# Performance work log

Measured on AMD Instinct MI355X. Metric: run time of the kernel, lower is better.

The kernel has to match this reference:

```python
import jax, jax.numpy as jnp
import numpy as np

B, L, D, E, K, P = 1024, 320, 128, 8, 2, 96
NOISE_EPS = 0.01
LOSS_COEF = 0.01


def setup_inputs() -> dict:
    key = jax.random.key(0)
    ks = jax.random.split(key, 8)
    return {
        "x": jax.random.normal(ks[0], (B, L, D), jnp.float32),
        "x_mark_enc": jax.random.normal(ks[1], (B, L, 4), jnp.float32),
        "noise": jax.random.normal(ks[2], (B, E), jnp.float32),  # randn_like in torch
        "start_w": jax.random.normal(ks[3], (D, 1), jnp.float32) * 0.05,
        "start_b": jnp.zeros((1,), jnp.float32),
        "w_gate": jax.random.normal(ks[4], (L, E), jnp.float32) * 0.02,
        "w_noise": jax.random.normal(ks[5], (L, E), jnp.float32) * 0.02,
        "expert_w": jax.random.normal(ks[6], (E, L, P), jnp.float32) * (1.0 / np.sqrt(L)),
        "expert_b": jnp.zeros((E, P, D), jnp.float32),
    }


def _norm_cdf(v):
    return 0.5 * (1.0 + jax.lax.erf(v * (1.0 / np.sqrt(2.0)).astype(v.dtype) if hasattr((1.0 / np.sqrt(2.0)), 'astype') else v / jnp.sqrt(jnp.asarray(2.0, v.dtype))))


def _cdf(v):
    # standard normal CDF, Normal(0,1).cdf
    return 0.5 * (1.0 + jax.lax.erf(v / jnp.sqrt(jnp.asarray(2.0, v.dtype))))


def _cv_squared(v):
    eps = 1e-10
    return jnp.var(v, ddof=1) / (jnp.mean(v) ** 2 + eps)


def reference(x, x_mark_enc, noise, start_w, start_b, w_gate, w_noise, expert_b, expert_w):
    # --- noisy top-k gating (train mode) ---
    g = jnp.squeeze(x @ start_w, -1) + start_b  # [B, L]
    clean_logits = g @ w_gate                    # [B, E]
    noise_std = jax.nn.softplus(g @ w_noise) + NOISE_EPS
    noisy_logits = clean_logits + noise * noise_std

    top_logits, top_idx = jax.lax.top_k(noisy_logits, K + 1)  # [B, K+1]
    top_k_gates = jax.nn.softmax(top_logits[:, :K], axis=1)
    gates = jnp.zeros_like(noisy_logits).at[
        jnp.arange(noisy_logits.shape[0])[:, None], top_idx[:, :K]
    ].set(top_k_gates)  # [B, E] sparse gates (zeros elsewhere)

    # --- differentiable load via prob-in-top-k ---
    thr_in = top_logits[:, K:K + 1]       # (k+1)-th noisy value
    thr_out = top_logits[:, K - 1:K]      # k-th noisy value
    clean_c = jnp.where(jnp.isnan(clean_logits), 0.0, clean_logits)
    prob = jnp.where(
        noisy_logits > thr_in,
        _cdf((clean_c - thr_in) / noise_std),
        _cdf((clean_c - thr_out) / noise_std),
    )
    load = prob.sum(0)          # [E]
    importance = gates.sum(0)   # [E]
    balance_loss = LOSS_COEF * (_cv_squared(importance) + _cv_squared(load))

    # --- dispatch/combine: dense-equivalent of SparseDispatcher ---
    # expert e: out_e = einsum('bld,lp->bpd', x, W_e); combine weights = gates
    per_expert = jnp.einsum('bld,elp->ebpd', x, expert_w)          # [E, B, P, D]
    out = jnp.einsum('be,ebpd->bpd', gates, per_expert)
    out = out + jnp.einsum('be,epd->bpd', gates, expert_b)
    regu_sum = jnp.asarray(0.0, jnp.float32)
    return out, balance_loss, regu_sum
```

## Files before the change

### kernel.cpp

```cpp
#include <hip/hip_runtime.h>
#include <hip/hip_bf16.h>

#define Bn 1024
#define Lr 320
#define Dd 128
#define Ee 8
#define Pp 96

typedef short bf16x8 __attribute__((ext_vector_type(8)));
typedef float f32x4 __attribute__((ext_vector_type(4)));
typedef unsigned u32x4 __attribute__((ext_vector_type(4)));
typedef unsigned short u16;

__device__ __forceinline__ float cdf_f(float v) {
    return 0.5f * (1.0f + erff(v * 0.70710678118654752f));
}
__device__ __forceinline__ float softplus_f(float x) {
    return fmaxf(x, 0.0f) + log1pf(expf(-fabsf(x)));
}
__device__ __forceinline__ u16 f2bf(float f) {
    unsigned int u = __float_as_uint(f);
    return (u16)((u + 0x7fffu + ((u >> 16) & 1u)) >> 16);
}
__device__ __forceinline__ float bf2f(u16 u) {
    return __uint_as_float(((unsigned int)u) << 16);
}

__device__ __forceinline__ void gload16(const void* g, void* l) {
    __builtin_amdgcn_global_load_lds(
        (const __attribute__((address_space(1))) void*)g,
        (__attribute__((address_space(3))) void*)l, 16, 0, 0);
}

__global__ __launch_bounds__(256) void transpose_w(
    const float* __restrict__ ew, u16* __restrict__ wt)
{
    __shared__ float tile[Pp * 33];
    const int e  = blockIdx.x;
    const int l0 = blockIdx.y * 32;
    const int t  = threadIdx.x;
    #pragma unroll
    for (int i = 0; i < 12; ++i) {
        const int idx = t + 256 * i;
        const int lp = idx / 96, p = idx - 96 * lp;
        tile[p * 33 + lp] = ew[((size_t)e * Lr + l0 + lp) * Pp + p];
    }
    __syncthreads();
    #pragma unroll
    for (int i = 0; i < 6; ++i) {
        const int g = t + 256 * i;
        const int p = g >> 4, l2 = (g & 15) * 2;
        const unsigned pk = (unsigned)f2bf(tile[p * 33 + l2]) |
                            ((unsigned)f2bf(tile[p * 33 + l2 + 1]) << 16);
        *(unsigned*)&wt[((size_t)(e * Pp + p)) * Lr + l0 + l2] = pk;
    }
}

__global__ __launch_bounds__(256, 8) void g_kernel(
    const float* __restrict__ x, const float* __restrict__ start_w,
    const float* __restrict__ start_b, float* __restrict__ g_out)
{
    const int t  = threadIdx.x;
    const int lc = blockIdx.x;
    const int b  = blockIdx.y;
    const float sb = start_b[0];

    float4 sw[4];
    #pragma unroll
    for (int j = 0; j < 4; ++j) sw[j] = ((const float4*)start_w)[(t & 7) + 8 * j];

    const float* xb = x + ((size_t)b * Lr + lc * 64) * Dd;
    #pragma unroll
    for (int p2 = 0; p2 < 2; ++p2) {
        const int r = p2 * 32 + (t >> 3);
        float acc = 0.f;
        #pragma unroll
        for (int j = 0; j < 4; ++j) {
            const float4 v = ((const float4*)(xb + (size_t)r * Dd))[(t & 7) + 8 * j];
            acc += v.x * sw[j].x + v.y * sw[j].y + v.z * sw[j].z + v.w * sw[j].w;
        }
        #pragma unroll
        for (int off = 1; off <= 4; off <<= 1) acc += __shfl_xor(acc, off);
        if ((t & 7) == 0) g_out[(size_t)b * Lr + lc * 64 + r] = acc + sb;
    }
}

__global__ __launch_bounds__(256) void gate_kernel(
    const float* __restrict__ g, const float* __restrict__ noise,
    const float* __restrict__ w_gate, const float* __restrict__ w_noise,
    float* __restrict__ accum, float* __restrict__ gates_out)
{
    __shared__ float sred[16];
    const int t    = threadIdx.x;
    const int lane = t & 63;
    const int wv   = t >> 6;
    const int b    = blockIdx.x * 4 + wv;

    if (t < 16) sred[t] = 0.f;
    __syncthreads();

    const int e = lane & 7, seg = lane >> 3;
    const float* gb = g + (size_t)b * Lr;
    float pc = 0.f, pn = 0.f;
    #pragma unroll 8
    for (int i = 0; i < 40; ++i) {
        const int l = seg * 40 + i;
        const float gv = gb[l];
        pc += gv * w_gate[l * Ee + e];
        pn += gv * w_noise[l * Ee + e];
    }
    #pragma unroll
    for (int off = 8; off <= 32; off <<= 1) {
        pc += __shfl_xor(pc, off);
        pn += __shfl_xor(pn, off);
    }
    const float sdv   = softplus_f(pn) + 0.01f;
    float       c     = pc;
    const float nz    = noise[b * Ee + e];
    const float noisy = c + nz * sdv;

    float nv[8];
    #pragma unroll
    for (int j = 0; j < 8; ++j) nv[j] = __shfl(noisy, j);

    int i0 = -1, i1 = -1;
    float v0 = -INFINITY, v1 = -INFINITY, v2 = -INFINITY;
    #pragma unroll
    for (int i = 0; i < 8; ++i) if (nv[i] > v0) { v0 = nv[i]; i0 = i; }
    #pragma unroll
    for (int i = 0; i < 8; ++i) if (i != i0 && nv[i] > v1) { v1 = nv[i]; i1 = i; }
    #pragma unroll
    for (int i = 0; i < 8; ++i) if (i != i0 && i != i1 && nv[i] > v2) { v2 = nv[i]; }

    const float ex1 = expf(v1 - v0);
    const float den = 1.f + ex1;
    const float gate_e = (e == i0) ? (1.f / den) : ((e == i1) ? (ex1 / den) : 0.f);

    if (isnan(c)) c = 0.f;
    const float pr = (noisy > v2) ? cdf_f((c - v2) / sdv) : cdf_f((c - v1) / sdv);

    if (lane < 8) {
        gates_out[b * Ee + e] = gate_e;
        atomicAdd(&sred[8 + e], gate_e);
        atomicAdd(&sred[e], pr);
    }
    __syncthreads();
    if (t < 16) atomicAdd(&accum[t], sred[t]);
}

__global__ __launch_bounds__(256, 4) void mm_kernel(
    const float* __restrict__ x, const u16* __restrict__ wt,
    const float* __restrict__ expert_b, const float* __restrict__ gates,
    float* __restrict__ out)
{
    __shared__ __align__(16) float    Xs[2][32 * 64];
    __shared__ __align__(16) unsigned Ws[2][192 * 16];

    const int b    = blockIdx.x >> 1;
    const int h    = blockIdx.x & 1;
    const int tid  = threadIdx.x;
    const int lane = tid & 63;
    const int wv   = tid >> 6;
    const int quad = lane >> 4;
    const int r16  = lane & 15;

    int e0 = 0, e1 = 0; float g0 = 0.f, g1 = 0.f; int cnt = 0;
    #pragma unroll
    for (int e = 0; e < Ee; ++e) {
        const float gv = gates[b * Ee + e];
        if (gv != 0.f) {
            if (cnt == 0) { e0 = e; g0 = gv; }
            else if (cnt == 1) { e1 = e; g1 = gv; }
            ++cnt;
        }
    }

    const float* xb  = x + (size_t)b * Lr * Dd + h * 64;
    const u16*   w0r = wt + (size_t)e0 * Pp * Lr;
    const u16*   w1r = wt + (size_t)e1 * Pp * Lr;

    const int xrow = lane >> 4;
    const int xcol = lane & 15;
    const int wrow = lane >> 2;
    const int wq   = lane & 3;

    auto STAGE = [&](int buf, int l0) {
        #pragma unroll
        for (int i = 0; i < 2; ++i) {
            const int c  = 2 * wv + i;
            const int l  = 4 * c + xrow;
            const int sx = (((l >> 3) & 1) << 4) | (((l >> 3) & 2) << 1);
            const int d4 = (4 * xcol) ^ sx;
            gload16(xb + (size_t)(l0 + l) * Dd + d4, (void*)&Xs[buf][c * 256]);
        }
        #pragma unroll
        for (int i = 0; i < 3; ++i) {
            const int c  = 3 * wv + i;
            const int r  = 16 * c + wrow;
            const int dw = (4 * wq) ^ ((r & 3) << 2);
            const u16* src = (c < 6) ? (w0r + (size_t)r * Lr)
                                     : (w1r + (size_t)(r - 96) * Lr);
            gload16(src + l0 + 2 * dw, (void*)&Ws[buf][c * 256]);
        }
    };

    f32x4 a0[6], a1[6];
    #pragma unroll
    for (int m = 0; m < 6; ++m) {
        a0[m] = (f32x4){0.f, 0.f, 0.f, 0.f};
        a1[m] = (f32x4){0.f, 0.f, 0.f, 0.f};
    }

    const int sxq    = ((quad & 1) << 4) | ((quad & 2) << 1);
    const int xcolr  = (16 * wv + r16) ^ sxq;
    const int wdw    = (4 * quad) ^ ((r16 & 3) << 2);

    union UF { u32x4 q; bf16x8 v; unsigned u[4]; };

    STAGE(0, 0);
    __syncthreads();
    int cur = 0;
    for (int t = 0; t < 10; ++t) {
        if (t < 9) STAGE(cur ^ 1, 32 * (t + 1));
        float xv[8];
        #pragma unroll
        for (int k = 0; k < 8; ++k)
            xv[k] = Xs[cur][(8 * quad + k) * 64 + xcolr];
        UF xf;
        #pragma unroll
        for (int k2 = 0; k2 < 4; ++k2)
            xf.u[k2] = (unsigned)f2bf(xv[2 * k2]) |
                       ((unsigned)f2bf(xv[2 * k2 + 1]) << 16);
        #pragma unroll
        for (int m = 0; m < 6; ++m) {
            UF a0f, a1f;
            a0f.q = *(const u32x4*)&Ws[cur][(16 * m + r16) * 16 + wdw];
            a1f.q = *(const u32x4*)&Ws[cur][(96 + 16 * m + r16) * 16 + wdw];
            a0[m] = __builtin_amdgcn_mfma_f32_16x16x32_bf16(a0f.v, xf.v, a0[m], 0, 0, 0);
            a1[m] = __builtin_amdgcn_mfma_f32_16x16x32_bf16(a1f.v, xf.v, a1[m], 0, 0, 0);
        }
        __syncthreads();
        cur ^= 1;
    }

    const int d = h * 64 + 16 * wv + r16;
    const float* eb0 = expert_b + (size_t)e0 * Pp * Dd;
    const float* eb1 = expert_b + (size_t)e1 * Pp * Dd;
    #pragma unroll
    for (int m = 0; m < 6; ++m) {
        #pragma unroll
        for (int r = 0; r < 4; ++r) {
            const int p = 16 * m + 4 * quad + r;
            out[((size_t)b * Pp + p) * Dd + d] =
                g0 * (a0[m][r] + eb0[p * Dd + d]) +
                g1 * (a1[m][r] + eb1[p * Dd + d]);
        }
    }
}

__global__ void loss_kernel(const float* __restrict__ accum,
                            float* __restrict__ out_scalars)
{
    if (threadIdx.x == 0) {
        float lo[8], im[8];
        #pragma unroll
        for (int i = 0; i < 8; ++i) { lo[i] = accum[i]; im[i] = accum[8 + i]; }
        float ml = 0.f, mi = 0.f;
        #pragma unroll
        for (int i = 0; i < 8; ++i) { ml += lo[i]; mi += im[i]; }
        ml *= 0.125f; mi *= 0.125f;
        float sl = 0.f, si = 0.f;
        #pragma unroll
        for (int i = 0; i < 8; ++i) {
            const float dl = lo[i] - ml, di = im[i] - mi;
            sl += dl * dl; si += di * di;
        }
        const float cvl = (sl / 7.f) / (ml * ml + 1e-10f);
        const float cvi = (si / 7.f) / (mi * mi + 1e-10f);
        out_scalars[0] = 0.01f * (cvi + cvl);
        out_scalars[1] = 0.0f;
    }
}

extern "C" void kernel_launch(void* const* d_in, const int* in_sizes, int n_in,
                              void* d_out, int out_size, void* d_ws, size_t ws_size,
                              hipStream_t stream)
{
    const float* x        = (const float*)d_in[0];
    const float* noise    = (const float*)d_in[2];
    const float* start_w  = (const float*)d_in[3];
    const float* start_b  = (const float*)d_in[4];
    const float* w_gate   = (const float*)d_in[5];
    const float* w_noise  = (const float*)d_in[6];
    const float* expert_w = (const float*)d_in[7];
    const float* expert_b = (const float*)d_in[8];
    float* out            = (float*)d_out;

    float* accum = (float*)d_ws;
    float* gates = accum + 16;
    float* gbuf  = gates + Bn * Ee;
    u16*   wt    = (u16*)(gbuf + Bn * Lr);

    hipMemsetAsync(accum, 0, 16 * sizeof(float), stream);
    hipLaunchKernelGGL(transpose_w, dim3(Ee, Lr / 32), dim3(256), 0, stream,
                       expert_w, wt);
    hipLaunchKernelGGL(g_kernel, dim3(5, Bn), dim3(256), 0, stream,
                       x, start_w, start_b, gbuf);
    hipLaunchKernelGGL(gate_kernel, dim3(Bn / 4), dim3(256), 0, stream,
                       gbuf, noise, w_gate, w_noise, accum, gates);
    hipLaunchKernelGGL(mm_kernel, dim3(Bn * 2), dim3(256), 0, stream,
                       x, wt, expert_b, gates, out);
    hipLaunchKernelGGL(loss_kernel, dim3(1), dim3(64), 0, stream,
                       accum, out + (size_t)Bn * Pp * Dd);
}
```

Before: 311.8 us.

## Fuse gating projection, top-k gating, and expert matmul into one per-batch kernel

Replaces the separate g, gate, and matmul kernels with one kernel per batch row. Each block reads the full x slab once, computes the start projection and the gating from it, and keeps a bf16-converted, transposed copy of x in LDS for the MFMA loop. This removes the second read of x from HBM, the global round-trips for g and gates, and two launches. In exchange each block needs about 80KB of LDS and 512 threads, which lowers occupancy. Global atomics now run per block instead of per four rows.

```diff
diff --git a/kernel.cpp b/kernel.cpp
--- a/kernel.cpp
+++ b/kernel.cpp
@@ -56,153 +56,147 @@
     }
 }
 
-__global__ __launch_bounds__(256, 8) void g_kernel(
-    const float* __restrict__ x, const float* __restrict__ start_w,
-    const float* __restrict__ start_b, float* __restrict__ g_out)
-{
-    const int t  = threadIdx.x;
-    const int lc = blockIdx.x;
-    const int b  = blockIdx.y;
-    const float sb = start_b[0];
-
-    float4 sw[4];
-    #pragma unroll
-    for (int j = 0; j < 4; ++j) sw[j] = ((const float4*)start_w)[(t & 7) + 8 * j];
-
-    const float* xb = x + ((size_t)b * Lr + lc * 64) * Dd;
-    #pragma unroll
-    for (int p2 = 0; p2 < 2; ++p2) {
-        const int r = p2 * 32 + (t >> 3);
-        float acc = 0.f;
-        #pragma unroll
-        for (int j = 0; j < 4; ++j) {
-            const float4 v = ((const float4*)(xb + (size_t)r * Dd))[(t & 7) + 8 * j];
-            acc += v.x * sw[j].x + v.y * sw[j].y + v.z * sw[j].z + v.w * sw[j].w;
-        }
-        #pragma unroll
-        for (int off = 1; off <= 4; off <<= 1) acc += __shfl_xor(acc, off);
-        if ((t & 7) == 0) g_out[(size_t)b * Lr + lc * 64 + r] = acc + sb;
-    }
-}
-
-__global__ __launch_bounds__(256) void gate_kernel(
-    const float* __restrict__ g, const float* __restrict__ noise,
+__global__ __launch_bounds__(512) void fused_kernel(
+    const float* __restrict__ x, const u16* __restrict__ wt,
+    const float* __restrict__ expert_b, const float* __restrict__ noise,
     const float* __restrict__ w_gate, const float* __restrict__ w_noise,
-    float* __restrict__ accum, float* __restrict__ gates_out)
-{
-    __shared__ float sred[16];
+    const float* __restrict__ start_w, const float* __restrict__ start_b,
+    float* __restrict__ accum, float* __restrict__ out)
+{
+    __shared__ __align__(16) unsigned XT[10 * 128 * 16];
+    __shared__ __align__(16) unsigned Ws[2][192 * 16];
+    __shared__ __align__(8)  float gl[Lr];
+    __shared__ float gsh[2];
+    __shared__ int   ish[2];
+
+    const int b    = blockIdx.x;
     const int t    = threadIdx.x;
     const int lane = t & 63;
     const int wv   = t >> 6;
-    const int b    = blockIdx.x * 4 + wv;
-
-    if (t < 16) sred[t] = 0.f;
-    __syncthreads();
-
-    const int e = lane & 7, seg = lane >> 3;
-    const float* gb = g + (size_t)b * Lr;
-    float pc = 0.f, pn = 0.f;
-    #pragma unroll 8
-    for (int i = 0; i < 40; ++i) {
-        const int l = seg * 40 + i;
-        const float gv = gb[l];
-        pc += gv * w_gate[l * Ee + e];
-        pn += gv * w_noise[l * Ee + e];
-    }
-    #pragma unroll
-    for (int off = 8; off <= 32; off <<= 1) {
-        pc += __shfl_xor(pc, off);
-        pn += __shfl_xor(pn, off);
-    }
-    const float sdv   = softplus_f(pn) + 0.01f;
-    float       c     = pc;
-    const float nz    = noise[b * Ee + e];
-    const float noisy = c + nz * sdv;
-
-    float nv[8];
-    #pragma unroll
-    for (int j = 0; j < 8; ++j) nv[j] = __shfl(noisy, j);
-
-    int i0 = -1, i1 = -1;
-    float v0 = -INFINITY, v1 = -INFINITY, v2 = -INFINITY;
-    #pragma unroll
-    for (int i = 0; i < 8; ++i) if (nv[i] > v0) { v0 = nv[i]; i0 = i; }
-    #pragma unroll
-    for (int i = 0; i < 8; ++i) if (i != i0 && nv[i] > v1) { v1 = nv[i]; i1 = i; }
-    #pragma unroll
-    for (int i = 0; i < 8; ++i) if (i != i0 && i != i1 && nv[i] > v2) { v2 = nv[i]; }
-
-    const float ex1 = expf(v1 - v0);
-    const float den = 1.f + ex1;
-    const float gate_e = (e == i0) ? (1.f / den) : ((e == i1) ? (ex1 / den) : 0.f);
-
-    if (isnan(c)) c = 0.f;
-    const float pr = (noisy > v2) ? cdf_f((c - v2) / sdv) : cdf_f((c - v1) / sdv);
-
-    if (lane < 8) {
-        gates_out[b * Ee + e] = gate_e;
-        atomicAdd(&sred[8 + e], gate_e);
-        atomicAdd(&sred[e], pr);
-    }
-    __syncthreads();
-    if (t < 16) atomicAdd(&accum[t], sred[t]);
-}
-
-__global__ __launch_bounds__(256, 4) void mm_kernel(
-    const float* __restrict__ x, const u16* __restrict__ wt,
-    const float* __restrict__ expert_b, const float* __restrict__ gates,
-    float* __restrict__ out)
-{
-    __shared__ __align__(16) float    Xs[2][32 * 64];
-    __shared__ __align__(16) unsigned Ws[2][192 * 16];
-
-    const int b    = blockIdx.x >> 1;
-    const int h    = blockIdx.x & 1;
-    const int tid  = threadIdx.x;
-    const int lane = tid & 63;
-    const int wv   = tid >> 6;
-    const int quad = lane >> 4;
-    const int r16  = lane & 15;
-
-    int e0 = 0, e1 = 0; float g0 = 0.f, g1 = 0.f; int cnt = 0;
-    #pragma unroll
-    for (int e = 0; e < Ee; ++e) {
-        const float gv = gates[b * Ee + e];
-        if (gv != 0.f) {
-            if (cnt == 0) { e0 = e; g0 = gv; }
-            else if (cnt == 1) { e1 = e; g1 = gv; }
-            ++cnt;
-        }
-    }
-
-    const float* xb  = x + (size_t)b * Lr * Dd + h * 64;
-    const u16*   w0r = wt + (size_t)e0 * Pp * Lr;
-    const u16*   w1r = wt + (size_t)e1 * Pp * Lr;
-
-    const int xrow = lane >> 4;
-    const int xcol = lane & 15;
-    const int wrow = lane >> 2;
-    const int wq   = lane & 3;
-
-    auto STAGE = [&](int buf, int l0) {
+
+    const float sb = start_b[0];
+    const int f8 = t & 7;
+    float4 sw[4];
+    #pragma unroll
+    for (int j = 0; j < 4; ++j) sw[j] = ((const float4*)start_w)[f8 + 8 * j];
+
+    #pragma unroll
+    for (int pass = 0; pass < 3; ++pass) {
+        const int pi = (t >> 3) + 64 * pass;
+        if (pi < 160) {
+            const float* r0 = x + ((size_t)b * Lr + 2 * pi) * Dd;
+            float4 v0[4], v1[4];
+            #pragma unroll
+            for (int j = 0; j < 4; ++j) {
+                v0[j] = ((const float4*)r0)[f8 + 8 * j];
+                v1[j] = ((const float4*)(r0 + Dd))[f8 + 8 * j];
+            }
+            float a0 = 0.f, a1 = 0.f;
+            #pragma unroll
+            for (int j = 0; j < 4; ++j) {
+                a0 += v0[j].x * sw[j].x + v0[j].y * sw[j].y +
+                      v0[j].z * sw[j].z + v0[j].w * sw[j].w;
+                a1 += v1[j].x * sw[j].x + v1[j].y * sw[j].y +
+                      v1[j].z * sw[j].z + v1[j].w * sw[j].w;
+            }
+            #pragma unroll
+            for (int off = 1; off <= 4; off <<= 1) {
+                a0 += __shfl_xor(a0, off);
+                a1 += __shfl_xor(a1, off);
+            }
+            if (f8 == 0) { gl[2 * pi] = a0 + sb; gl[2 * pi + 1] = a1 + sb; }
+            const int tt = pi >> 4, k2 = pi & 15;
+            #pragma unroll
+            for (int j = 0; j < 4; ++j) {
+                const float* p0 = (const float*)&v0[j];
+                const float* p1 = (const float*)&v1[j];
+                #pragma unroll
+                for (int jj = 0; jj < 4; ++jj) {
+                    const int d  = 4 * (f8 + 8 * j) + jj;
+                    const int sg = ((d ^ (d >> 2)) & 3) << 2;
+                    XT[(tt * 128 + d) * 16 + (k2 ^ sg)] =
+                        (unsigned)f2bf(p0[jj]) | ((unsigned)f2bf(p1[jj]) << 16);
+                }
+            }
+        }
+    }
+    __syncthreads();
+
+    if (t < 64) {
+        const int e = t & 7, seg = t >> 3;
+        float pc = 0.f, pn = 0.f;
+        #pragma unroll 8
+        for (int i = 0; i < 40; ++i) {
+            const int l = seg * 40 + i;
+            const float gv = gl[l];
+            pc += gv * w_gate[l * Ee + e];
+            pn += gv * w_noise[l * Ee + e];
+        }
+        #pragma unroll
+        for (int off = 8; off <= 32; off <<= 1) {
+            pc += __shfl_xor(pc, off);
+            pn += __shfl_xor(pn, off);
+        }
+        const float sdv   = softplus_f(pn) + 0.01f;
+        float       c     = pc;
+        const float nz    = noise[b * Ee + e];
+        const float noisy = c + nz * sdv;
+
+        float nv[8];
+        #pragma unroll
+        for (int j = 0; j < 8; ++j) nv[j] = __shfl(noisy, j);
+
+        int i0 = -1, i1 = -1;
+        float v0 = -INFINITY, v1 = -INFINITY, v2 = -INFINITY;
+        #pragma unroll
+        for (int i = 0; i < 8; ++i) if (nv[i] > v0) { v0 = nv[i]; i0 = i; }
+        #pragma unroll
+        for (int i = 0; i < 8; ++i) if (i != i0 && nv[i] > v1) { v1 = nv[i]; i1 = i; }
+        #pragma unroll
+        for (int i = 0; i < 8; ++i) if (i != i0 && i != i1 && nv[i] > v2) { v2 = nv[i]; }
+
+        const float ex1 = expf(v1 - v0);
+        const float den = 1.f + ex1;
+        const float gate_e = (e == i0) ? (1.f / den) : ((e == i1) ? (ex1 / den) : 0.f);
+
+        if (isnan(c)) c = 0.f;
+        const float pr = (noisy > v2) ? cdf_f((c - v2) / sdv) : cdf_f((c - v1) / sdv);
+
+        if (t == 0) {
+            ish[0] = i0; ish[1] = i1;
+            gsh[0] = 1.f / den; gsh[1] = ex1 / den;
+        }
+        if (t < 8) {
+            atomicAdd(&accum[8 + e], gate_e);
+            atomicAdd(&accum[e], pr);
+        }
+    }
+    __syncthreads();
+
+    const int e0 = ish[0], e1 = ish[1];
+    const float g0 = gsh[0], g1 = gsh[1];
+    const u16* w0r = wt + (size_t)e0 * Pp * Lr;
+    const u16* w1r = wt + (size_t)e1 * Pp * Lr;
+
+    const int wrow = lane >> 2, wq = lane & 3;
+    auto STAGE_W = [&](int buf, int l0) {
         #pragma unroll
         for (int i = 0; i < 2; ++i) {
-            const int c  = 2 * wv + i;
-            const int l  = 4 * c + xrow;
-            const int sx = (((l >> 3) & 1) << 4) | (((l >> 3) & 2) << 1);
-            const int d4 = (4 * xcol) ^ sx;
-            gload16(xb + (size_t)(l0 + l) * Dd + d4, (void*)&Xs[buf][c * 256]);
-        }
-        #pragma unroll
-        for (int i = 0; i < 3; ++i) {
-            const int c  = 3 * wv + i;
-            const int r  = 16 * c + wrow;
-            const int dw = (4 * wq) ^ ((r & 3) << 2);
-            const u16* src = (c < 6) ? (w0r + (size_t)r * Lr)
-                                     : (w1r + (size_t)(r - 96) * Lr);
-            gload16(src + l0 + 2 * dw, (void*)&Ws[buf][c * 256]);
+            const int c = wv + 8 * i;
+            if (c < 12) {
+                const int r  = 16 * c + wrow;
+                const int dw = (4 * wq) ^ ((r & 3) << 2);
+                const u16* src = (c < 6) ? (w0r + (size_t)r * Lr)
+                                         : (w1r + (size_t)(r - 96) * Lr);
+                gload16(src + l0 + 2 * dw, (void*)&Ws[buf][c * 256]);
+            }
         }
     };
+
+    const int quad = lane >> 4, r16 = lane & 15;
+    const int xdw  = 4 * (quad ^ ((r16 ^ (r16 >> 2)) & 3));
+    const int wdw  = (4 * quad) ^ ((r16 & 3) << 2);
+    const int xrow = (16 * wv + r16) * 16;
 
     f32x4 a0[6], a1[6];
     #pragma unroll
@@ -211,39 +205,28 @@
         a1[m] = (f32x4){0.f, 0.f, 0.f, 0.f};
     }
 
-    const int sxq    = ((quad & 1) << 4) | ((quad & 2) << 1);
-    const int xcolr  = (16 * wv + r16) ^ sxq;
-    const int wdw    = (4 * quad) ^ ((r16 & 3) << 2);
-
-    union UF { u32x4 q; bf16x8 v; unsigned u[4]; };
-
-    STAGE(0, 0);
+    union UF { u32x4 q; bf16x8 v; };
+
+    STAGE_W(0, 0);
     __syncthreads();
     int cur = 0;
-    for (int t = 0; t < 10; ++t) {
-        if (t < 9) STAGE(cur ^ 1, 32 * (t + 1));
-        float xv[8];
-        #pragma unroll
-        for (int k = 0; k < 8; ++k)
-            xv[k] = Xs[cur][(8 * quad + k) * 64 + xcolr];
+    for (int kt = 0; kt < 10; ++kt) {
+        if (kt < 9) STAGE_W(cur ^ 1, 32 * (kt + 1));
         UF xf;
-        #pragma unroll
-        for (int k2 = 0; k2 < 4; ++k2)
-            xf.u[k2] = (unsigned)f2bf(xv[2 * k2]) |
-                       ((unsigned)f2bf(xv[2 * k2 + 1]) << 16);
+        xf.q = *(const u32x4*)&XT[kt * 2048 + xrow + xdw];
         #pragma unroll
         for (int m = 0; m < 6; ++m) {
-            UF a0f, a1f;
-            a0f.q = *(const u32x4*)&Ws[cur][(16 * m + r16) * 16 + wdw];
-            a1f.q = *(const u32x4*)&Ws[cur][(96 + 16 * m + r16) * 16 + wdw];
-            a0[m] = __builtin_amdgcn_mfma_f32_16x16x32_bf16(a0f.v, xf.v, a0[m], 0, 0, 0);
-            a1[m] = __builtin_amdgcn_mfma_f32_16x16x32_bf16(a1f.v, xf.v, a1[m], 0, 0, 0);
+            UF f0, f1;
+            f0.q = *(const u32x4*)&Ws[cur][(16 * m + r16) * 16 + wdw];
+            f1.q = *(const u32x4*)&Ws[cur][(96 + 16 * m + r16) * 16 + wdw];
+            a0[m] = __builtin_amdgcn_mfma_f32_16x16x32_bf16(f0.v, xf.v, a0[m], 0, 0, 0);
+            a1[m] = __builtin_amdgcn_mfma_f32_16x16x32_bf16(f1.v, xf.v, a1[m], 0, 0, 0);
         }
         __syncthreads();
         cur ^= 1;
     }
 
-    const int d = h * 64 + 16 * wv + r16;
+    const int d = 16 * wv + r16;
     const float* eb0 = expert_b + (size_t)e0 * Pp * Dd;
     const float* eb1 = expert_b + (size_t)e1 * Pp * Dd;
     #pragma unroll
@@ -297,19 +280,14 @@
     float* out            = (float*)d_out;
 
     float* accum = (float*)d_ws;
-    float* gates = accum + 16;
-    float* gbuf  = gates + Bn * Ee;
-    u16*   wt    = (u16*)(gbuf + Bn * Lr);
+    u16*   wt    = (u16*)((char*)d_ws + 256);
 
     hipMemsetAsync(accum, 0, 16 * sizeof(float), stream);
     hipLaunchKernelGGL(transpose_w, dim3(Ee, Lr / 32), dim3(256), 0, stream,
                        expert_w, wt);
-    hipLaunchKernelGGL(g_kernel, dim3(5, Bn), dim3(256), 0, stream,
-                       x, start_w, start_b, gbuf);
-    hipLaunchKernelGGL(gate_kernel, dim3(Bn / 4), dim3(256), 0, stream,
-                       gbuf, noise, w_gate, w_noise, accum, gates);
-    hipLaunchKernelGGL(mm_kernel, dim3(Bn * 2), dim3(256), 0, stream,
-                       x, wt, expert_b, gates, out);
+    hipLaunchKernelGGL(fused_kernel, dim3(Bn), dim3(512), 0, stream,
+                       x, wt, expert_b, noise, w_gate, w_noise,
+                       start_w, start_b, accum, out);
     hipLaunchKernelGGL(loss_kernel, dim3(1), dim3(64), 0, stream,
                        accum, out + (size_t)Bn * Pp * Dd);
 }
```

After: 313.5 us. About the same (+0.5%).

## Drop memset and loss launch, load x directly into registers in mm_kernel

Applied to the files above, without the earlier changes.

The accumulator zeroing moves into the transpose kernel, and the loss computation is folded into block 0 of mm_kernel, which removes a memset and a separate kernel launch. mm_kernel stops staging x through LDS. Each thread now loads its own x values from global memory into registers, with a manually unrolled two-buffer schedule, while W is still staged through LDS with async loads. This cuts LDS traffic and shared-memory footprint, but the direct x loads are strided per-thread reads that may coalesce less well than the earlier 16-byte LDS-direct loads.

```diff
diff --git a/kernel.cpp b/kernel.cpp
--- a/kernel.cpp
+++ b/kernel.cpp
@@ -33,12 +33,14 @@
 }
 
 __global__ __launch_bounds__(256) void transpose_w(
-    const float* __restrict__ ew, u16* __restrict__ wt)
+    const float* __restrict__ ew, u16* __restrict__ wt,
+    float* __restrict__ accum)
 {
     __shared__ float tile[Pp * 33];
     const int e  = blockIdx.x;
     const int l0 = blockIdx.y * 32;
     const int t  = threadIdx.x;
+    if (e == 0 && blockIdx.y == 0 && t < 16) accum[t] = 0.f;
     #pragma unroll
     for (int i = 0; i < 12; ++i) {
         const int idx = t + 256 * i;
@@ -151,14 +153,35 @@
 __global__ __launch_bounds__(256, 4) void mm_kernel(
     const float* __restrict__ x, const u16* __restrict__ wt,
     const float* __restrict__ expert_b, const float* __restrict__ gates,
-    float* __restrict__ out)
-{
-    __shared__ __align__(16) float    Xs[2][32 * 64];
+    const float* __restrict__ accum, float* __restrict__ out)
+{
     __shared__ __align__(16) unsigned Ws[2][192 * 16];
+
+    const int tid  = threadIdx.x;
+
+    if (blockIdx.x == 0 && tid == 0) {
+        float lo[8], im[8];
+        #pragma unroll
+        for (int i = 0; i < 8; ++i) { lo[i] = accum[i]; im[i] = accum[8 + i]; }
+        float ml = 0.f, mi = 0.f;
+        #pragma unroll
+        for (int i = 0; i < 8; ++i) { ml += lo[i]; mi += im[i]; }
+        ml *= 0.125f; mi *= 0.125f;
+        float sl = 0.f, si = 0.f;
+        #pragma unroll
+        for (int i = 0; i < 8; ++i) {
+            const float dl = lo[i] - ml, di = im[i] - mi;
+            sl += dl * dl; si += di * di;
+        }
+        const float cvl = (sl / 7.f) / (ml * ml + 1e-10f);
+        const float cvi = (si / 7.f) / (mi * mi + 1e-10f);
+        float* os = out + (size_t)Bn * Pp * Dd;
+        os[0] = 0.01f * (cvi + cvl);
+        os[1] = 0.0f;
+    }
 
     const int b    = blockIdx.x >> 1;
     const int h    = blockIdx.x & 1;
-    const int tid  = threadIdx.x;
     const int lane = tid & 63;
     const int wv   = tid >> 6;
     const int quad = lane >> 4;
@@ -175,24 +198,16 @@
         }
     }
 
-    const float* xb  = x + (size_t)b * Lr * Dd + h * 64;
-    const u16*   w0r = wt + (size_t)e0 * Pp * Lr;
-    const u16*   w1r = wt + (size_t)e1 * Pp * Lr;
-
-    const int xrow = lane >> 4;
-    const int xcol = lane & 15;
+    const u16* w0r = wt + (size_t)e0 * Pp * Lr;
+    const u16* w1r = wt + (size_t)e1 * Pp * Lr;
+
+    const int d = h * 64 + 16 * wv + r16;
+    const float* xg = x + ((size_t)b * Lr + 8 * quad) * Dd + d;
+
     const int wrow = lane >> 2;
     const int wq   = lane & 3;
 
-    auto STAGE = [&](int buf, int l0) {
-        #pragma unroll
-        for (int i = 0; i < 2; ++i) {
-            const int c  = 2 * wv + i;
-            const int l  = 4 * c + xrow;
-            const int sx = (((l >> 3) & 1) << 4) | (((l >> 3) & 2) << 1);
-            const int d4 = (4 * xcol) ^ sx;
-            gload16(xb + (size_t)(l0 + l) * Dd + d4, (void*)&Xs[buf][c * 256]);
-        }
+    auto STAGE_W = [&](int buf, int l0) {
         #pragma unroll
         for (int i = 0; i < 3; ++i) {
             const int c  = 3 * wv + i;
@@ -204,6 +219,13 @@
         }
     };
 
+    float xa[8], xb8[8];
+    auto LOADX = [&](float* dst, int l0) {
+        #pragma unroll
+        for (int k = 0; k < 8; ++k)
+            dst[k] = xg[(size_t)(l0 + k) * Dd];
+    };
+
     f32x4 a0[6], a1[6];
     #pragma unroll
     for (int m = 0; m < 6; ++m) {
@@ -211,21 +233,11 @@
         a1[m] = (f32x4){0.f, 0.f, 0.f, 0.f};
     }
 
-    const int sxq    = ((quad & 1) << 4) | ((quad & 2) << 1);
-    const int xcolr  = (16 * wv + r16) ^ sxq;
-    const int wdw    = (4 * quad) ^ ((r16 & 3) << 2);
+    const int wdw = (4 * quad) ^ ((r16 & 3) << 2);
 
     union UF { u32x4 q; bf16x8 v; unsigned u[4]; };
 
-    STAGE(0, 0);
-    __syncthreads();
-    int cur = 0;
-    for (int t = 0; t < 10; ++t) {
-        if (t < 9) STAGE(cur ^ 1, 32 * (t + 1));
-        float xv[8];
-        #pragma unroll
-        for (int k = 0; k < 8; ++k)
-            xv[k] = Xs[cur][(8 * quad + k) * 64 + xcolr];
+    auto COMPUTE = [&](int buf, const float* xv) {
         UF xf;
         #pragma unroll
         for (int k2 = 0; k2 < 4; ++k2)
@@ -233,17 +245,32 @@
                        ((unsigned)f2bf(xv[2 * k2 + 1]) << 16);
         #pragma unroll
         for (int m = 0; m < 6; ++m) {
-            UF a0f, a1f;
-            a0f.q = *(const u32x4*)&Ws[cur][(16 * m + r16) * 16 + wdw];
-            a1f.q = *(const u32x4*)&Ws[cur][(96 + 16 * m + r16) * 16 + wdw];
-            a0[m] = __builtin_amdgcn_mfma_f32_16x16x32_bf16(a0f.v, xf.v, a0[m], 0, 0, 0);
-            a1[m] = __builtin_amdgcn_mfma_f32_16x16x32_bf16(a1f.v, xf.v, a1[m], 0, 0, 0);
-        }
+            UF f0, f1;
+            f0.q = *(const u32x4*)&Ws[buf][(16 * m + r16) * 16 + wdw];
+            f1.q = *(const u32x4*)&Ws[buf][(96 + 16 * m + r16) * 16 + wdw];
+            a0[m] = __builtin_amdgcn_mfma_f32_16x16x32_bf16(f0.v, xf.v, a0[m], 0, 0, 0);
+            a1[m] = __builtin_amdgcn_mfma_f32_16x16x32_bf16(f1.v, xf.v, a1[m], 0, 0, 0);
+        }
+    };
+
+    STAGE_W(0, 0);
+    LOADX(xa, 0);
+    __syncthreads();
+
+    #pragma unroll
+    for (int t = 0; t < 10; t += 2) {
+        STAGE_W(1, 32 * (t + 1));
+        LOADX(xb8, 32 * (t + 1));
+        COMPUTE(0, xa);
         __syncthreads();
-        cur ^= 1;
-    }
-
-    const int d = h * 64 + 16 * wv + r16;
+        if (t + 2 < 10) {
+            STAGE_W(0, 32 * (t + 2));
+            LOADX(xa, 32 * (t + 2));
+        }
+        COMPUTE(1, xb8);
+        __syncthreads();
+    }
+
     const float* eb0 = expert_b + (size_t)e0 * Pp * Dd;
     const float* eb1 = expert_b + (size_t)e1 * Pp * Dd;
     #pragma unroll
@@ -255,30 +282,6 @@
                 g0 * (a0[m][r] + eb0[p * Dd + d]) +
                 g1 * (a1[m][r] + eb1[p * Dd + d]);
         }
-    }
-}
-
-__global__ void loss_kernel(const float* __restrict__ accum,
-                            float* __restrict__ out_scalars)
-{
-    if (threadIdx.x == 0) {
-        float lo[8], im[8];
-        #pragma unroll
-        for (int i = 0; i < 8; ++i) { lo[i] = accum[i]; im[i] = accum[8 + i]; }
-        float ml = 0.f, mi = 0.f;
-        #pragma unroll
-        for (int i = 0; i < 8; ++i) { ml += lo[i]; mi += im[i]; }
-        ml *= 0.125f; mi *= 0.125f;
-        float sl = 0.f, si = 0.f;
-        #pragma unroll
-        for (int i = 0; i < 8; ++i) {
-            const float dl = lo[i] - ml, di = im[i] - mi;
-            sl += dl * dl; si += di * di;
-        }
-        const float cvl = (sl / 7.f) / (ml * ml + 1e-10f);
-        const float cvi = (si / 7.f) / (mi * mi + 1e-10f);
-        out_scalars[0] = 0.01f * (cvi + cvl);
-        out_scalars[1] = 0.0f;
     }
 }
 
@@ -301,15 +304,12 @@
     float* gbuf  = gates + Bn * Ee;
     u16*   wt    = (u16*)(gbuf + Bn * Lr);
 
-    hipMemsetAsync(accum, 0, 16 * sizeof(float), stream);
     hipLaunchKernelGGL(transpose_w, dim3(Ee, Lr / 32), dim3(256), 0, stream,
-                       expert_w, wt);
+                       expert_w, wt, accum);
     hipLaunchKernelGGL(g_kernel, dim3(5, Bn), dim3(256), 0, stream,
                        x, start_w, start_b, gbuf);
     hipLaunchKernelGGL(gate_kernel, dim3(Bn / 4), dim3(256), 0, stream,
                        gbuf, noise, w_gate, w_noise, accum, gates);
     hipLaunchKernelGGL(mm_kernel, dim3(Bn * 2), dim3(256), 0, stream,
-                       x, wt, expert_b, gates, out);
-    hipLaunchKernelGGL(loss_kernel, dim3(1), dim3(64), 0, stream,
-                       accum, out + (size_t)Bn * Pp * Dd);
-}
+                       x, wt, expert_b, gates, accum, out);
+}
```

After: 304.8 us. 2.2% less time.
